# Kernel tuning notes

Hardware: AMD Instinct MI355X
Metric: run time of the kernel (lower is better)

The kernel has to match this reference:

```python
import jax, jax.numpy as jnp
import numpy as np

SCALES = (64, 64, 64)  # matches init_kwargs


def setup_inputs() -> dict:
    key = jax.random.key(0)
    B, N = 64, 65536
    # points uniform in [-1, 1)^3, as assumed by GRNet gridding
    ptcloud = jax.random.uniform(key, (B, N, 3), dtype=jnp.float32, minval=-1.0, maxval=1.0)
    return {"ptcloud": ptcloud}


def reference(ptcloud):
    sx, sy, sz = SCALES
    B, N, _ = ptcloud.shape
    dtype = ptcloud.dtype

    scale_factors = jnp.array([sx / 2.0, sy / 2.0, sz / 2.0], dtype=dtype)
    p = ptcloud * scale_factors  # (B, N, 3) in [-s/2, s/2)

    # replicate the per-sample filtering of all-zero (padding) points:
    # zero points contribute nothing to the grid
    nz_mask = jnp.sum(jnp.abs(p), axis=-1) != 0  # (B, N)

    lower = jnp.floor(p)          # lower corner coordinate
    frac = p - lower              # trilinear fractional offsets, (B, N, 3)
    half = jnp.array([sx // 2, sy // 2, sz // 2], jnp.int32)
    lower_i = lower.astype(jnp.int32) + half  # shift from [-s/2, s/2) to grid index [0, s)

    # 8 corner offsets of the enclosing voxel cell
    offsets = jnp.array([[i, j, k] for i in (0, 1) for j in (0, 1) for k in (0, 1)], jnp.int32)  # (8, 3)
    idx = lower_i[:, :, None, :] + offsets  # (B, N, 8, 3)

    dims = jnp.array([sx, sy, sz], jnp.int32)
    in_bounds = jnp.all((idx >= 0) & (idx < dims), axis=-1)  # (B, N, 8)

    # trilinear weight: prod over dims of (1-frac) for lower corner, frac for upper
    f = frac[:, :, None, :]  # (B, N, 1, 3)
    w3 = jnp.where(offsets[None, None] == 0, 1.0 - f, f)  # (B, N, 8, 3)
    w = jnp.prod(w3, axis=-1)  # (B, N, 8)
    w = w * (in_bounds & nz_mask[:, :, None]).astype(dtype)

    idx_c = jnp.clip(idx, 0, dims - 1)  # safe indices (masked-out weights are zero)
    b_idx = jnp.arange(B, dtype=jnp.int32)[:, None, None]
    flat = ((b_idx * sx + idx_c[..., 0]) * sy + idx_c[..., 1]) * sz + idx_c[..., 2]  # (B, N, 8)

    grid = jnp.zeros(B * sx * sy * sz, dtype=dtype).at[flat.reshape(-1)].add(w.reshape(-1))
    return grid.reshape(B, sx * sy * sz)
```

## Files before the change

### kernel.cpp

```cpp
#include <hip/hip_runtime.h>


#define NPTS   65536
#define NCHUNK 32
#define CHSZ   2048
#define NSLAB  16
#define SLABW  4
#define CCAP   256
#define SLOTS  (NCHUNK * CCAP)
#define ACCN   16384
#define QSCALE 262144.0f
#define QINV   (1.0f / 262144.0f)

__global__ __launch_bounds__(512) void p1_bin(
    const float* __restrict__ pt,
    float* __restrict__ gx, float* __restrict__ gy, float* __restrict__ gz,
    int* __restrict__ bcnt)
{
    __shared__ float sxl[NSLAB * CCAP];
    __shared__ float syl[NSLAB * CCAP];
    __shared__ float szl[NSLAB * CCAP];
    __shared__ int   cnt[NSLAB];
    if (threadIdx.x < NSLAB) cnt[threadIdx.x] = 0;
    __syncthreads();

    const int blk = blockIdx.x;
    const int b = blk >> 5;
    const int c = blk & 31;
    const float* p = pt + ((size_t)b * NPTS + (size_t)c * CHSZ) * 3;

    #pragma unroll
    for (int k = 0; k < CHSZ / 512; ++k) {
        int li = k * 512 + threadIdx.x;
        float px = p[3 * li + 0] * 32.0f;
        float py = p[3 * li + 1] * 32.0f;
        float pz = p[3 * li + 2] * 32.0f;
        if (fabsf(px) + fabsf(py) + fabsf(pz) == 0.0f) continue;
        int ix = (int)floorf(px) + 32;
        if ((unsigned)ix > 63u) continue;
        int s0 = ix >> 2;
        int pos = atomicAdd(&cnt[s0], 1);
        if (pos < CCAP) {
            int a = s0 * CCAP + pos;
            sxl[a] = px; syl[a] = py; szl[a] = pz;
        }
        if ((ix & 3) == 3 && ix < 63) {
            int pos1 = atomicAdd(&cnt[s0 + 1], 1);
            if (pos1 < CCAP) {
                int a = (s0 + 1) * CCAP + pos1;
                sxl[a] = px; syl[a] = py; szl[a] = pz;
            }
        }
    }
    __syncthreads();

    #pragma unroll
    for (int i = threadIdx.x; i < NSLAB * CCAP; i += 512) {
        int s = i >> 8, e = i & 255;
        size_t d = ((size_t)((b * NSLAB + s) * NCHUNK + c)) * CCAP + e;
        gx[d] = sxl[i]; gy[d] = syl[i]; gz[d] = szl[i];
    }
    if (threadIdx.x < NSLAB)
        bcnt[(b * NSLAB + threadIdx.x) * NCHUNK + c] = min(cnt[threadIdx.x], CCAP);
}

__device__ __forceinline__ void accum_corners(
    unsigned int* S, float px, float py, float pz, int x0)
{
    float lx = floorf(px), ly = floorf(py), lz = floorf(pz);
    float fx = px - lx,    fy = py - ly,    fz = pz - lz;
    int ix = (int)lx + 32, iy = (int)ly + 32, iz = (int)lz + 32;
    if ((unsigned)iz > 63u) return;

    float wx[2] = {1.0f - fx, fx};
    float wy[2] = {1.0f - fy, fy};
    float wz0 = 1.0f - fz, wz1 = fz;

    const int odd = iz & 1;
    const int zoff = odd ? (ACCN + iz - 1) : iz;
    const bool hi_ok = (iz != 63);

    #pragma unroll
    for (int di = 0; di < 2; ++di) {
        int xl = ix + di - x0;
        if ((unsigned)xl >= 2u) continue;
        #pragma unroll
        for (int dj = 0; dj < 2; ++dj) {
            int yy = iy + dj;
            if ((unsigned)yy >= 64u) continue;
            float wxy = wx[di] * wy[dj];
            unsigned int q0 = __float2uint_rn(wxy * wz0 * QSCALE);
            unsigned int q1 = hi_ok ? __float2uint_rn(wxy * wz1 * QSCALE) : 0u;
            int cb = (xl * 64 + yy) * 64;
            unsigned long long pk =
                (unsigned long long)q0 | ((unsigned long long)q1 << 32);
            atomicAdd((unsigned long long*)&S[cb + zoff], pk);
        }
    }
}

__global__ __launch_bounds__(1024) void p2_accum(
    const float* __restrict__ gx, const float* __restrict__ gy,
    const float* __restrict__ gz, const int* __restrict__ bcnt,
    const float* __restrict__ pt, float* __restrict__ out)
{
    __shared__ unsigned int S[2 * ACCN];
    __shared__ int rescan;

    const int pb = blockIdx.x >> 1;
    const int h  = blockIdx.x & 1;
    const int b  = pb >> 4;
    const int s  = pb & 15;
    const int x0 = s * SLABW + h * 2;

    if (threadIdx.x == 0) rescan = 0;
    uint4* s4 = (uint4*)S;
    #pragma unroll
    for (int i = threadIdx.x; i < (2 * ACCN) / 4; i += 1024)
        s4[i] = make_uint4(0u, 0u, 0u, 0u);
    __syncthreads();

    if (threadIdx.x < NCHUNK) {
        if ((unsigned)bcnt[pb * NCHUNK + threadIdx.x] >= (unsigned)CCAP)
            rescan = 1;
    }
    __syncthreads();

    if (!rescan) {
        const size_t base = (size_t)pb * SLOTS;
        const int* myc = bcnt + pb * NCHUNK;

        #pragma unroll
        for (int t = threadIdx.x; t < SLOTS; t += 1024) {
            int c = t >> 8;
            int pos = t & 255;
            if (pos >= myc[c]) continue;
            float px = gx[base + t];
            float py = gy[base + t];
            float pz = gz[base + t];
            accum_corners(S, px, py, pz, x0);
        }
    } else {
        const float* p = pt + (size_t)b * NPTS * 3;
        for (int i = threadIdx.x; i < NPTS; i += 1024) {
            float px = p[3 * i + 0] * 32.0f;
            float py = p[3 * i + 1] * 32.0f;
            float pz = p[3 * i + 2] * 32.0f;
            if (fabsf(px) + fabsf(py) + fabsf(pz) == 0.0f) continue;
            accum_corners(S, px, py, pz, x0);
        }
    }
    __syncthreads();

    float* o = out + ((size_t)b * 64 + x0) * 4096;
    #pragma unroll
    for (int i = threadIdx.x; i < 2 * 4096; i += 1024) {
        int z = i & 63;
        unsigned int v = S[i] + (z ? S[ACCN + i - 1] : 0u);
        o[i] = (float)v * QINV;
    }
}

__global__ __launch_bounds__(1024) void gridding_slab(
    const float* __restrict__ pt, float* __restrict__ out)
{
    __shared__ float lds[SLABW * 64 * 64];
    const int blk = blockIdx.x;
    const int b   = blk >> 4;
    const int x0  = (blk & 15) * SLABW;
    float4* l4 = (float4*)lds;
    #pragma unroll
    for (int i = threadIdx.x; i < (SLABW * 64 * 64) / 4; i += 1024)
        l4[i] = make_float4(0.f, 0.f, 0.f, 0.f);
    __syncthreads();
    const float* p = pt + (size_t)b * NPTS * 3;
    for (int it = 0; it < NPTS / 1024; ++it) {
        int i = it * 1024 + threadIdx.x;
        float px = p[3 * i + 0] * 32.0f;
        float py = p[3 * i + 1] * 32.0f;
        float pz = p[3 * i + 2] * 32.0f;
        if (fabsf(px) + fabsf(py) + fabsf(pz) == 0.0f) continue;
        float lx = floorf(px), ly = floorf(py), lz = floorf(pz);
        float fx = px - lx, fy = py - ly, fz = pz - lz;
        int ix = (int)lx + 32, iy = (int)ly + 32, iz = (int)lz + 32;
        float wx[2] = {1.0f - fx, fx};
        float wy[2] = {1.0f - fy, fy};
        float wz[2] = {1.0f - fz, fz};
        #pragma unroll
        for (int di = 0; di < 2; ++di) {
            int xl = (ix + di) - x0;
            if ((unsigned)xl >= SLABW) continue;
            #pragma unroll
            for (int dj = 0; dj < 2; ++dj) {
                int yy = iy + dj;
                if ((unsigned)yy >= 64u) continue;
                float wxy = wx[di] * wy[dj];
                int basei = (xl * 64 + yy) * 64;
                #pragma unroll
                for (int dk = 0; dk < 2; ++dk) {
                    int zz = iz + dk;
                    if ((unsigned)zz >= 64u) continue;
                    atomicAdd(&lds[basei + zz], wxy * wz[dk]);
                }
            }
        }
    }
    __syncthreads();
    float4* o4 = (float4*)(out + ((size_t)b * 64 + x0) * 4096);
    #pragma unroll
    for (int i = threadIdx.x; i < (SLABW * 64 * 64) / 4; i += 1024)
        o4[i] = l4[i];
}

extern "C" void kernel_launch(void* const* d_in, const int* in_sizes, int n_in,
                              void* d_out, int out_size, void* d_ws, size_t ws_size,
                              hipStream_t stream) {
    const float* pt = (const float*)d_in[0];
    float* out = (float*)d_out;
    const int B = (in_sizes[0] / 3) / NPTS;

    const size_t nbuck = (size_t)B * NSLAB;
    const size_t arr   = nbuck * SLOTS;
    const size_t need  = 3 * arr * sizeof(float) + nbuck * NCHUNK * sizeof(int);

    if (ws_size >= need) {
        float* gx = (float*)d_ws;
        float* gy = gx + arr;
        float* gz = gy + arr;
        int* bcnt = (int*)(gz + arr);
        p1_bin<<<B * NCHUNK, 512, 0, stream>>>(pt, gx, gy, gz, bcnt);
        p2_accum<<<(int)(nbuck * 2), 1024, 0, stream>>>(gx, gy, gz, bcnt, pt, out);
    } else {
        gridding_slab<<<B * NSLAB, 1024, 0, stream>>>(pt, out);
    }
}
```

Baseline: 192.5 us.

## Pack binned points into 64-bit fixed-point words and store only occupied slots

The binning pass now quantizes each point's shifted coordinates to 21-bit fixed point (6 integer bits, 15 fraction bits) and packs all three into a single 64-bit word. The intermediate buffer therefore takes 8 bytes per point instead of 12, split across three float arrays. Writeback is restricted to filled slots, so unused capacity is no longer written. The accumulation pass reads one word and decodes cell index and fraction with shifts and masks, at the cost of quantizing the fractional weights to 1/32768, which may slightly change results.

Result: faster. 174.7 us (-9.2%).

```diff
diff --git a/kernel.cpp b/kernel.cpp
--- a/kernel.cpp
+++ b/kernel.cpp
@@ -11,16 +11,17 @@
 #define ACCN   16384
 #define QSCALE 262144.0f
 #define QINV   (1.0f / 262144.0f)
+#define CMASK  0x1FFFFFu
+#define FSCALE 32768.0f
+#define FINV   (1.0f / 32768.0f)
 
 __global__ __launch_bounds__(512) void p1_bin(
     const float* __restrict__ pt,
-    float* __restrict__ gx, float* __restrict__ gy, float* __restrict__ gz,
+    unsigned long long* __restrict__ gp,
     int* __restrict__ bcnt)
 {
-    __shared__ float sxl[NSLAB * CCAP];
-    __shared__ float syl[NSLAB * CCAP];
-    __shared__ float szl[NSLAB * CCAP];
-    __shared__ int   cnt[NSLAB];
+    __shared__ unsigned long long spk[NSLAB * CCAP];
+    __shared__ int cnt[NSLAB];
     if (threadIdx.x < NSLAB) cnt[threadIdx.x] = 0;
     __syncthreads();
 
@@ -36,20 +37,19 @@
         float py = p[3 * li + 1] * 32.0f;
         float pz = p[3 * li + 2] * 32.0f;
         if (fabsf(px) + fabsf(py) + fabsf(pz) == 0.0f) continue;
-        int ix = (int)floorf(px) + 32;
-        if ((unsigned)ix > 63u) continue;
+        unsigned ux = min(__float2uint_rn((px + 32.0f) * FSCALE), CMASK);
+        unsigned uy = min(__float2uint_rn((py + 32.0f) * FSCALE), CMASK);
+        unsigned uz = min(__float2uint_rn((pz + 32.0f) * FSCALE), CMASK);
+        int ix = (int)(ux >> 15);
+        unsigned long long pk =
+            (unsigned long long)ux | ((unsigned long long)uy << 21)
+                                   | ((unsigned long long)uz << 42);
         int s0 = ix >> 2;
         int pos = atomicAdd(&cnt[s0], 1);
-        if (pos < CCAP) {
-            int a = s0 * CCAP + pos;
-            sxl[a] = px; syl[a] = py; szl[a] = pz;
-        }
+        if (pos < CCAP) spk[s0 * CCAP + pos] = pk;
         if ((ix & 3) == 3 && ix < 63) {
             int pos1 = atomicAdd(&cnt[s0 + 1], 1);
-            if (pos1 < CCAP) {
-                int a = (s0 + 1) * CCAP + pos1;
-                sxl[a] = px; syl[a] = py; szl[a] = pz;
-            }
+            if (pos1 < CCAP) spk[(s0 + 1) * CCAP + pos1] = pk;
         }
     }
     __syncthreads();
@@ -57,19 +57,19 @@
     #pragma unroll
     for (int i = threadIdx.x; i < NSLAB * CCAP; i += 512) {
         int s = i >> 8, e = i & 255;
-        size_t d = ((size_t)((b * NSLAB + s) * NCHUNK + c)) * CCAP + e;
-        gx[d] = sxl[i]; gy[d] = syl[i]; gz[d] = szl[i];
+        if (e < min(cnt[s], CCAP)) {
+            size_t d = ((size_t)((b * NSLAB + s) * NCHUNK + c)) * CCAP + e;
+            gp[d] = spk[i];
+        }
     }
     if (threadIdx.x < NSLAB)
         bcnt[(b * NSLAB + threadIdx.x) * NCHUNK + c] = min(cnt[threadIdx.x], CCAP);
 }
 
 __device__ __forceinline__ void accum_corners(
-    unsigned int* S, float px, float py, float pz, int x0)
-{
-    float lx = floorf(px), ly = floorf(py), lz = floorf(pz);
-    float fx = px - lx,    fy = py - ly,    fz = pz - lz;
-    int ix = (int)lx + 32, iy = (int)ly + 32, iz = (int)lz + 32;
+    unsigned int* S, int ix, int iy, int iz,
+    float fx, float fy, float fz, int x0)
+{
     if ((unsigned)iz > 63u) return;
 
     float wx[2] = {1.0f - fx, fx};
@@ -100,8 +100,7 @@
 }
 
 __global__ __launch_bounds__(1024) void p2_accum(
-    const float* __restrict__ gx, const float* __restrict__ gy,
-    const float* __restrict__ gz, const int* __restrict__ bcnt,
+    const unsigned long long* __restrict__ gp, const int* __restrict__ bcnt,
     const float* __restrict__ pt, float* __restrict__ out)
 {
     __shared__ unsigned int S[2 * ACCN];
@@ -135,10 +134,14 @@
             int c = t >> 8;
             int pos = t & 255;
             if (pos >= myc[c]) continue;
-            float px = gx[base + t];
-            float py = gy[base + t];
-            float pz = gz[base + t];
-            accum_corners(S, px, py, pz, x0);
+            unsigned long long pk = gp[base + t];
+            unsigned ux = (unsigned)pk & CMASK;
+            unsigned uy = (unsigned)(pk >> 21) & CMASK;
+            unsigned uz = (unsigned)(pk >> 42) & CMASK;
+            accum_corners(S, (int)(ux >> 15), (int)(uy >> 15), (int)(uz >> 15),
+                          (float)(ux & 32767u) * FINV,
+                          (float)(uy & 32767u) * FINV,
+                          (float)(uz & 32767u) * FINV, x0);
         }
     } else {
         const float* p = pt + (size_t)b * NPTS * 3;
@@ -147,7 +150,11 @@
             float py = p[3 * i + 1] * 32.0f;
             float pz = p[3 * i + 2] * 32.0f;
             if (fabsf(px) + fabsf(py) + fabsf(pz) == 0.0f) continue;
-            accum_corners(S, px, py, pz, x0);
+            float gxs = px + 32.0f, gys = py + 32.0f, gzs = pz + 32.0f;
+            float lx = floorf(gxs), ly = floorf(gys), lz = floorf(gzs);
+            int ix = (int)lx, iy = (int)ly, iz = (int)lz;
+            if ((unsigned)ix > 63u) continue;
+            accum_corners(S, ix, iy, iz, gxs - lx, gys - ly, gzs - lz, x0);
         }
     }
     __syncthreads();
@@ -221,15 +228,14 @@
 
     const size_t nbuck = (size_t)B * NSLAB;
     const size_t arr   = nbuck * SLOTS;
-    const size_t need  = 3 * arr * sizeof(float) + nbuck * NCHUNK * sizeof(int);
+    const size_t need  = arr * sizeof(unsigned long long)
+                       + nbuck * NCHUNK * sizeof(int);
 
     if (ws_size >= need) {
-        float* gx = (float*)d_ws;
-        float* gy = gx + arr;
-        float* gz = gy + arr;
-        int* bcnt = (int*)(gz + arr);
-        p1_bin<<<B * NCHUNK, 512, 0, stream>>>(pt, gx, gy, gz, bcnt);
-        p2_accum<<<(int)(nbuck * 2), 1024, 0, stream>>>(gx, gy, gz, bcnt, pt, out);
+        unsigned long long* gp = (unsigned long long*)d_ws;
+        int* bcnt = (int*)(gp + arr);
+        p1_bin<<<B * NCHUNK, 512, 0, stream>>>(pt, gp, bcnt);
+        p2_accum<<<(int)(nbuck * 2), 1024, 0, stream>>>(gp, bcnt, pt, out);
     } else {
         gridding_slab<<<B * NSLAB, 1024, 0, stream>>>(pt, out);
     }
```
